# Kernel optimization log

Measured on AMD Instinct MI355X. Metric: run time of the kernel, lower is better.

## Reference

```python
import jax, jax.numpy as jnp
import numpy as np

B, T, I, E, K, J = 4, 4096, 1024, 16, 512, 1024

def setup_inputs() -> dict:
    key = jax.random.key(0)
    k1, k2, k3 = jax.random.split(key, 3)
    X = jax.random.normal(k1, (B, T, I), dtype=jnp.float32)
    ind = jax.random.randint(k2, (B, E, K), 0, T, dtype=jnp.int64)
    W = jax.random.normal(k3, (E, I, J), dtype=jnp.float32)
    return {"X": X, "ind": ind, "W": W}

def reference(X, ind, W):
    b, t, i = X.shape
    # offset each batch's indices into the flattened [B*T, I] token table
    offset = jnp.arange(b, dtype=ind.dtype)[:, None, None] * t  # [B,1,1]
    X_flat = X.reshape(b * t, i)
    X_gathered = X_flat[ind + offset]  # [B,E,K,I] irregular gather
    Y = jnp.einsum('beki,eij->bekj', X_gathered, W)  # grouped GEMM per expert
    return Y
```

## Files before the change

### kernel.cpp

```cpp
#include <hip/hip_runtime.h>

#define DI __device__ __forceinline__

constexpr int Bc = 4, Tc = 4096, Ic = 1024, Ec = 16, Kc = 512, Jc = 1024;

typedef __attribute__((ext_vector_type(8))) short short8;
typedef __attribute__((ext_vector_type(4))) float floatx4;

DI unsigned pack2_bf16(float a, float b) {
  union { float f; unsigned u; } ua, ub;
  ua.f = a; ub.f = b;
  const unsigned x = ua.u + 0x8000u;
  const unsigned y = ub.u + 0x8000u;
#if __has_builtin(__builtin_amdgcn_perm)
  return __builtin_amdgcn_perm(y, x, 0x07060302u);
#else
  return (x >> 16) | (y & 0xFFFF0000u);
#endif
}

DI void async_load16(const void* g, void* lds) {
  __builtin_amdgcn_global_load_lds((const __attribute__((address_space(1))) void*)g,
                                   (__attribute__((address_space(3))) void*)lds,
                                   16, 0, 0);
}

__global__ __launch_bounds__(256) void prep(const float* __restrict__ X,
                                            const int* __restrict__ ind,
                                            const float* __restrict__ W,
                                            unsigned short* __restrict__ Xg,
                                            unsigned short* __restrict__ Wt) {
  __shared__ __align__(16) char smem[32 * 260 * 2];
  const int bid = blockIdx.x >> 1;
  const int t = threadIdx.x;

  if ((blockIdx.x & 1) == 0) {
    unsigned short* Ls = (unsigned short*)smem;
    const int g = t >> 5, kk = t & 31;
    const int R = bid * 8 + g;
    const int b = R >> 13;
    const int xr = ind[R];
    const float* src = X + ((size_t)(b * Tc + xr)) * Ic + kk * 32;
    unsigned u[16];
#pragma unroll
    for (int q = 0; q < 8; ++q) {
      const float4 v = *(const float4*)(src + q * 4);
      u[2 * q]     = pack2_bf16(v.x, v.y);
      u[2 * q + 1] = pack2_bf16(v.z, v.w);
    }
    unsigned short* lp = &Ls[kk * 260 + g * 32];
#pragma unroll
    for (int q = 0; q < 4; ++q) *(uint4*)(lp + q * 8) = *(uint4*)&u[4 * q];
    __syncthreads();
    const int kk2 = t >> 3, rw = t & 7;
    const int tt = bid >> 4;
    const int rl0 = (bid & 15) * 8;
    unsigned short* dst = Xg + ((size_t)(tt * 32 + kk2) * 128 + rl0 + rw) * 32;
    const unsigned short* lr = &Ls[kk2 * 260 + rw * 32];
#pragma unroll
    for (int q = 0; q < 4; ++q) *(uint4*)(dst + q * 8) = *(const uint4*)(lr + q * 8);
  } else {
    float (*tile)[129] = (float(*)[129])smem;
    const int kk = bid & 31;
    const int jt = (bid >> 5) & 7;
    const int e  = bid >> 8;
    const float* Wp = W + ((size_t)(e * Ic + kk * 32)) * Jc + jt * 128;
#pragma unroll
    for (int p = 0; p < 4; ++p) {
      const int il = p * 8 + (t >> 5);
      const int c4 = (t & 31) * 4;
      const float4 v = *(const float4*)(Wp + (size_t)il * Jc + c4);
      tile[il][c4 + 0] = v.x; tile[il][c4 + 1] = v.y;
      tile[il][c4 + 2] = v.z; tile[il][c4 + 3] = v.w;
    }
    __syncthreads();
    unsigned short* out = Wt + ((size_t)((e * 8 + jt) * 32 + kk)) * 4096;
#pragma unroll
    for (int h = 0; h < 2; ++h) {
      const int n   = h * 64 + (t >> 2);
      const int il0 = (t & 3) * 8;
      unsigned u[4];
#pragma unroll
      for (int q = 0; q < 4; ++q)
        u[q] = pack2_bf16(tile[il0 + 2 * q][n], tile[il0 + 2 * q + 1][n]);
      *(uint4*)(out + (size_t)(h * 256 + t) * 8) = *(uint4*)u;
    }
  }
}

__global__ __launch_bounds__(512, 2) void moe_gemm(const unsigned short* __restrict__ Xg,
                                                   const unsigned short* __restrict__ Wt,
                                                   float* __restrict__ Y) {
  __shared__ __align__(16) unsigned short As[4 * 8192];
  __shared__ __align__(16) unsigned short Bs[4 * 8192];

  const int bid   = blockIdx.x;
  const int lg    = (bid & 7) * 64 + (bid >> 3);
  const int e     = lg >> 5;
  const int inner = lg & 31;
  const int b     = inner >> 3;
  const int mt    = (inner >> 2) & 1;
  const int nt    = inner & 3;

  const int t = threadIdx.x;
  const int w = t >> 6;
  const int l = t & 63;
  const int lrow = l & 15;
  const int q    = l >> 4;

  const int tt0 = b * 64 + e * 4 + mt * 2;
  const int jg0 = e * 8 + nt * 2;

  const int sr = t >> 2, sc = t & 3;
  const size_t lsrc = (size_t)sr * 32 + ((sc ^ ((sr >> 1) & 3)) << 3);

  const unsigned short* aC = Xg + (size_t)tt0 * 32 * 4096 + lsrc;
  const unsigned short* bC = Wt + (size_t)jg0 * 32 * 4096 + lsrc;
  unsigned short* aL = As + w * 512;
  unsigned short* bL = Bs + w * 512;

  auto stage = [&](int k3) {
    const int bu = (k3 & 3) * 8192;
#pragma unroll
    for (int p = 0; p < 2; ++p) {
      async_load16(aC + ((size_t)(p * 32 + k3)) * 4096, aL + bu + p * 4096);
      async_load16(bC + ((size_t)(p * 32 + k3)) * 4096, bL + bu + p * 4096);
    }
  };

  floatx4 acc[8][4];
#pragma unroll
  for (int tm = 0; tm < 8; ++tm)
#pragma unroll
    for (int tn = 0; tn < 4; ++tn) acc[tm][tn] = (floatx4){0.f, 0.f, 0.f, 0.f};

  const int pos = (q ^ ((lrow >> 1) & 3)) << 3;
  const unsigned short* Ard = As + ((w >> 2) << 12) + lrow * 32 + pos;
  const unsigned short* Brd = Bs + (((w >> 1) & 1) << 12) + ((w & 1) * 64 + lrow) * 32 + pos;

  stage(0); stage(1); stage(2);

  auto compute = [&](int kt) {
    const int bu = (kt & 3) * 8192;
    short8 bf[4];
#pragma unroll
    for (int tn = 0; tn < 4; ++tn) bf[tn] = *(const short8*)(Brd + bu + tn * 512);
    __builtin_amdgcn_s_setprio(1);
#pragma unroll
    for (int h = 0; h < 2; ++h) {
      short8 af[4];
#pragma unroll
      for (int i2 = 0; i2 < 4; ++i2)
        af[i2] = *(const short8*)(Ard + bu + (h * 4 + i2) * 512);
#pragma unroll
      for (int i2 = 0; i2 < 4; ++i2)
#pragma unroll
        for (int tn = 0; tn < 4; ++tn)
          acc[h * 4 + i2][tn] =
              __builtin_amdgcn_mfma_f32_16x16x32_bf16(af[i2], bf[tn], acc[h * 4 + i2][tn], 0, 0, 0);
    }
    __builtin_amdgcn_s_setprio(0);
  };

#define WAITVM(n) asm volatile("s_waitcnt vmcnt(" #n ")" ::: "memory")
#define CFENCE    asm volatile("" ::: "memory")

#pragma unroll 4
  for (int kt = 0; kt < 28; ++kt) {
    WAITVM(8);
    __builtin_amdgcn_s_barrier();
    CFENCE;
    stage(kt + 3);
    compute(kt);
  }
  WAITVM(8); __builtin_amdgcn_s_barrier(); CFENCE; stage(31); compute(28);
  WAITVM(8); __builtin_amdgcn_s_barrier(); CFENCE; compute(29);
  WAITVM(4); __builtin_amdgcn_s_barrier(); CFENCE; compute(30);
  WAITVM(0); __builtin_amdgcn_s_barrier(); CFENCE; compute(31);

  float* Yp = Y + (((size_t)(b * Ec + e) * Kc + (size_t)mt * 256) * Jc) + nt * 256;
  const int wmRow = (w >> 2) * 128;
  const int wnCol = (w & 3) * 64;
#pragma unroll
  for (int tm = 0; tm < 8; ++tm) {
#pragma unroll
    for (int tn = 0; tn < 4; ++tn) {
#pragma unroll
      for (int r = 0; r < 4; ++r) {
        const int row = wmRow + tm * 16 + q * 4 + r;
        const int col = wnCol + tn * 16 + lrow;
        Yp[(size_t)row * Jc + col] = acc[tm][tn][r];
      }
    }
  }
}

extern "C" void kernel_launch(void* const* d_in, const int* in_sizes, int n_in,
                              void* d_out, int out_size, void* d_ws, size_t ws_size,
                              hipStream_t stream) {
  const float* X = (const float*)d_in[0];
  const int* ind = (const int*)d_in[1];
  const float* W = (const float*)d_in[2];
  float* Y = (float*)d_out;

  unsigned short* Xg = (unsigned short*)d_ws;
  unsigned short* Wt = (unsigned short*)d_ws + (size_t)Bc * Ec * Kc * Ic;

  hipLaunchKernelGGL(prep, dim3(8192), dim3(256), 0, stream, X, ind, W, Xg, Wt);
  hipLaunchKernelGGL(moe_gemm, dim3(512), dim3(512), 0, stream, Xg, Wt, Y);
}
```

Measured before the change: 327.7 us.

## Remove LDS staging from prep kernel; write gathered X and transposed W directly

The prep kernel no longer stages X rows or W tiles through shared memory with a barrier. Each thread now converts its slice to bf16 and writes it straight to the tiled workspace layout. The W transpose instead does strided scalar column reads, 32 rows apart by Jc, which coalesce across threads along n. The grid shrinks from 8192 to 6144 blocks. This removes LDS traffic and syncs, but the X writes become 64-byte chunks per thread with a different coalescing pattern, and the W reads become scalar.

```diff
diff --git a/kernel.cpp b/kernel.cpp
--- a/kernel.cpp
+++ b/kernel.cpp
@@ -30,16 +30,19 @@
                                             const float* __restrict__ W,
                                             unsigned short* __restrict__ Xg,
                                             unsigned short* __restrict__ Wt) {
-  __shared__ __align__(16) char smem[32 * 260 * 2];
-  const int bid = blockIdx.x >> 1;
   const int t = threadIdx.x;
+  const int bx = blockIdx.x;
 
-  if ((blockIdx.x & 1) == 0) {
-    unsigned short* Ls = (unsigned short*)smem;
-    const int g = t >> 5, kk = t & 31;
-    const int R = bid * 8 + g;
-    const int b = R >> 13;
-    const int xr = ind[R];
+  if (bx < 4096) {
+    const int item = bx * 256 + t;
+    const int rl6 = item & 63;
+    const int rh  = (item >> 6) & 1;
+    const int kk  = (item >> 7) & 31;
+    const int tt  = item >> 12;
+    const int rl  = rh * 64 + rl6;
+    const int R   = tt * 128 + rl;
+    const int b   = R >> 13;
+    const int xr  = ind[R];
     const float* src = X + ((size_t)(b * Tc + xr)) * Ic + kk * 32;
     unsigned u[16];
 #pragma unroll
@@ -48,43 +51,27 @@
       u[2 * q]     = pack2_bf16(v.x, v.y);
       u[2 * q + 1] = pack2_bf16(v.z, v.w);
     }
-    unsigned short* lp = &Ls[kk * 260 + g * 32];
+    unsigned short* dst = Xg + ((size_t)((tt * 32 + kk) * 128 + rl)) * 32;
 #pragma unroll
-    for (int q = 0; q < 4; ++q) *(uint4*)(lp + q * 8) = *(uint4*)&u[4 * q];
-    __syncthreads();
-    const int kk2 = t >> 3, rw = t & 7;
-    const int tt = bid >> 4;
-    const int rl0 = (bid & 15) * 8;
-    unsigned short* dst = Xg + ((size_t)(tt * 32 + kk2) * 128 + rl0 + rw) * 32;
-    const unsigned short* lr = &Ls[kk2 * 260 + rw * 32];
+    for (int q = 0; q < 4; ++q) *(uint4*)(dst + q * 8) = *(uint4*)&u[4 * q];
+  } else {
+    const int item = (bx - 4096) * 256 + t;
+    const int n   = item & 127;
+    const int grp = item >> 7;
+    const int kk  = grp & 31;
+    const int jt  = (grp >> 5) & 7;
+    const int e   = grp >> 8;
+    const float* src = W + ((size_t)(e * Ic + kk * 32)) * Jc + jt * 128 + n;
+    unsigned u[16];
 #pragma unroll
-    for (int q = 0; q < 4; ++q) *(uint4*)(dst + q * 8) = *(const uint4*)(lr + q * 8);
-  } else {
-    float (*tile)[129] = (float(*)[129])smem;
-    const int kk = bid & 31;
-    const int jt = (bid >> 5) & 7;
-    const int e  = bid >> 8;
-    const float* Wp = W + ((size_t)(e * Ic + kk * 32)) * Jc + jt * 128;
+    for (int q = 0; q < 16; ++q) {
+      const float a = src[(size_t)(2 * q) * Jc];
+      const float c = src[(size_t)(2 * q + 1) * Jc];
+      u[q] = pack2_bf16(a, c);
+    }
+    unsigned short* dst = Wt + (size_t)grp * 4096 + n * 32;
 #pragma unroll
-    for (int p = 0; p < 4; ++p) {
-      const int il = p * 8 + (t >> 5);
-      const int c4 = (t & 31) * 4;
-      const float4 v = *(const float4*)(Wp + (size_t)il * Jc + c4);
-      tile[il][c4 + 0] = v.x; tile[il][c4 + 1] = v.y;
-      tile[il][c4 + 2] = v.z; tile[il][c4 + 3] = v.w;
-    }
-    __syncthreads();
-    unsigned short* out = Wt + ((size_t)((e * 8 + jt) * 32 + kk)) * 4096;
-#pragma unroll
-    for (int h = 0; h < 2; ++h) {
-      const int n   = h * 64 + (t >> 2);
-      const int il0 = (t & 3) * 8;
-      unsigned u[4];
-#pragma unroll
-      for (int q = 0; q < 4; ++q)
-        u[q] = pack2_bf16(tile[il0 + 2 * q][n], tile[il0 + 2 * q + 1][n]);
-      *(uint4*)(out + (size_t)(h * 256 + t) * 8) = *(uint4*)u;
-    }
+    for (int q = 0; q < 4; ++q) *(uint4*)(dst + q * 8) = *(uint4*)&u[4 * q];
   }
 }
 
@@ -206,6 +193,6 @@
   unsigned short* Xg = (unsigned short*)d_ws;
   unsigned short* Wt = (unsigned short*)d_ws + (size_t)Bc * Ec * Kc * Ic;
 
-  hipLaunchKernelGGL(prep, dim3(8192), dim3(256), 0, stream, X, ind, W, Xg, Wt);
+  hipLaunchKernelGGL(prep, dim3(6144), dim3(256), 0, stream, X, ind, W, Xg, Wt);
   hipLaunchKernelGGL(moe_gemm, dim3(512), dim3(512), 0, stream, Xg, Wt, Y);
 }
```

Result: no change. 328.9 us (+0.4%).
